# Kernel optimization log

Measured on AMD Instinct MI355X. Metric: run time of the kernel, lower is better.

Reference implementation:

```python
import jax, jax.numpy as jnp
import numpy as np

K = 512          # fixed candidate budget (replaces dynamic torch.where)
THRESH = 0.6
IOU = 0.5
STRIDE = 2.0
OFFSET = 6.0
WIN = 12.0
SCALE = 0.6      # pyramid scale this pass represents (12/min_face_size)


def _conv(x, w, b):
    y = jax.lax.conv_general_dilated(x, w, (1, 1), 'VALID',
                                     dimension_numbers=('NCHW', 'OIHW', 'NCHW'))
    return y + b[None, :, None, None]


def _prelu(x, a):
    return jnp.where(x >= 0, x, a[None, :, None, None] * x)


def _maxpool2(x):
    return jax.lax.reduce_window(x, -jnp.inf, jax.lax.max,
                                 (1, 1, 2, 2), (1, 1, 2, 2), 'VALID')


def _nms(boxes, valid, thr):
    # torchvision-style greedy NMS over score-sorted boxes; `valid` marks live boxes.
    x1, y1, x2, y2 = boxes[:, 0], boxes[:, 1], boxes[:, 2], boxes[:, 3]
    areas = (x2 - x1) * (y2 - y1)
    n = boxes.shape[0]
    idxs = jnp.arange(n)

    def body(i, keep):
        xi1 = jnp.maximum(x1[i], x1); yi1 = jnp.maximum(y1[i], y1)
        xi2 = jnp.minimum(x2[i], x2); yi2 = jnp.minimum(y2[i], y2)
        inter = jnp.clip(xi2 - xi1, 0.0) * jnp.clip(yi2 - yi1, 0.0)
        iou = inter / (areas[i] + areas - inter + 1e-9)
        sup = (iou > thr) & (idxs > i) & keep[i]
        return keep & (~sup)

    return jax.lax.fori_loop(0, n, body, valid)


def setup_inputs() -> dict:
    key = jax.random.key(0)
    ks = jax.random.split(key, 14)
    d = {}
    d['x'] = jax.random.normal(ks[0], (1, 3, 2048, 2048), dtype=jnp.float32)
    d['w1'] = jax.random.normal(ks[1], (10, 3, 3, 3), dtype=jnp.float32) * 0.1
    d['b1'] = jax.random.normal(ks[2], (10,), dtype=jnp.float32) * 0.01
    d['p1'] = jax.random.uniform(ks[3], (10,), dtype=jnp.float32) * 0.25
    d['w2'] = jax.random.normal(ks[4], (16, 10, 3, 3), dtype=jnp.float32) * 0.1
    d['b2'] = jax.random.normal(ks[5], (16,), dtype=jnp.float32) * 0.01
    d['p2'] = jax.random.uniform(ks[6], (16,), dtype=jnp.float32) * 0.25
    d['w3'] = jax.random.normal(ks[7], (32, 16, 3, 3), dtype=jnp.float32) * 0.1
    d['b3'] = jax.random.normal(ks[8], (32,), dtype=jnp.float32) * 0.01
    d['p3'] = jax.random.uniform(ks[9], (32,), dtype=jnp.float32) * 0.25
    d['wa'] = jax.random.normal(ks[10], (2, 32, 1, 1), dtype=jnp.float32) * 0.1
    d['ba'] = jax.random.normal(ks[11], (2,), dtype=jnp.float32) * 0.01
    d['wb'] = jax.random.normal(ks[12], (4, 32, 1, 1), dtype=jnp.float32) * 0.1
    d['bb'] = jax.random.normal(ks[13], (4,), dtype=jnp.float32) * 0.01
    return d


def reference(x, w1, b1, p1, w2, b2, p2, w3, b3, p3, wa, ba, wb, bb):
    H, W = x.shape[2], x.shape[3]
    h = _prelu(_conv(x, w1, b1), p1)
    h = _maxpool2(h)
    h = _prelu(_conv(h, w2, b2), p2)
    h = _prelu(_conv(h, w3, b3), p3)
    cls = _conv(h, wa, ba)              # [1,2,hf,wf]
    reg = _conv(h, wb, bb)              # [1,4,hf,wf]
    prob = jax.nn.softmax(cls, axis=1)[0, 1]   # Softmax2d over channels, face prob
    hf, wf = prob.shape
    scores = prob.reshape(-1)
    regf = jnp.transpose(reg[0], (1, 2, 0)).reshape(-1, 4)
    # threshold gather -> fixed-size top-K with invalid slots at score -1
    masked = jnp.where(scores >= THRESH, scores, -1.0)
    top_s, idx = jax.lax.top_k(masked, K)
    reg_k = regf[idx]
    yy = (idx // wf).astype(jnp.float32)
    xx = (idx % wf).astype(jnp.float32)
    off_x = ((W - OFFSET * 2) % STRIDE) / 2.0 + OFFSET
    off_y = ((H - OFFSET * 2) % STRIDE) / 2.0 + OFFSET
    cx = (xx * STRIDE + off_x) / SCALE
    cy = (yy * STRIDE + off_y) / SCALE
    ww = WIN / SCALE                    # square 12x12 window / scale
    x1 = cx - ww / 2 + reg_k[:, 0] * ww
    y1 = cy - ww / 2 + reg_k[:, 1] * ww
    x2 = cx + ww / 2 + reg_k[:, 2] * ww
    y2 = cy + ww / 2 + reg_k[:, 3] * ww
    boxes = jnp.stack([x1, y1, x2, y2], axis=1)   # [K,4]
    valid = top_s >= THRESH
    keep = _nms(boxes, valid, IOU)                # per-scale NMS
    keep = _nms(boxes, keep, IOU + 0.2)           # final cross-scale NMS
    out = jnp.concatenate([boxes, top_s[:, None]], axis=1)
    return out * keep[:, None].astype(out.dtype)  # [K,5] boxes+score, zeroed if dropped
```

## Files before the change

### kernel.cpp

```cpp
#include <hip/hip_runtime.h>

typedef unsigned long long u64;
typedef unsigned int u32;

#define W1H 1023
#define W2H 1021
#define W3H 1019
#define NPIX (W3H * W3H)
#define IDXMASK 0xFFFFFull
#define PSTR 1024

#define NBINS 2048
#define HLO 0.3055f
#define HW_ 0.025f
#define HINV 40.0f
#define HDELTA 0.10f

#define W1OFF 0
#define B1OFF 270
#define P1OFF 280
#define W2OFF 290
#define B2OFF 1730
#define P2OFF 1746
#define W3OFF 1762
#define B3OFF 6370
#define P3OFF 6402
#define WAOFF 6434
#define BAOFF 6498
#define WBOFF 6500
#define BBOFF 6628
#define WDTOT 6632

__device__ __forceinline__ int xcd_swizzle(int bid, int nwg) {
    int q = nwg >> 3, r = nwg & 7;
    int x = bid & 7, i = bid >> 3;
    return (x < r ? x * (q + 1) : r * (q + 1) + (x - r) * q) + i;
}

__global__ __launch_bounds__(256) void k_prep(
    const float* __restrict__ w1, const float* __restrict__ b1, const float* __restrict__ p1,
    const float* __restrict__ w2, const float* __restrict__ b2, const float* __restrict__ p2,
    const float* __restrict__ w3, const float* __restrict__ b3, const float* __restrict__ p3,
    const float* __restrict__ wa, const float* __restrict__ ba,
    const float* __restrict__ wb, const float* __restrict__ bb,
    double* __restrict__ wd, int* __restrict__ ctrl, u32* __restrict__ ghist)
{
    int t = threadIdx.x;
    if (t < 2) ctrl[t] = 0;
    for (int i = t; i < NBINS; i += 256) ghist[i] = 0u;
    for (int i = t; i < 270; i += 256)  wd[W1OFF + i] = (double)w1[i];
    if (t < 10) { wd[B1OFF + t] = (double)b1[t]; wd[P1OFF + t] = (double)p1[t]; }
    for (int i = t; i < 1440; i += 256) wd[W2OFF + i] = (double)w2[i];
    if (t < 16) { wd[B2OFF + t] = (double)b2[t]; wd[P2OFF + t] = (double)p2[t]; }
    for (int i = t; i < 4608; i += 256) wd[W3OFF + i] = (double)w3[i];
    if (t < 32) { wd[B3OFF + t] = (double)b3[t]; wd[P3OFF + t] = (double)p3[t]; }
    if (t < 64)  wd[WAOFF + t] = (double)wa[t];
    if (t < 2)   wd[BAOFF + t] = (double)ba[t];
    if (t < 128) wd[WBOFF + t] = (double)wb[t];
    if (t < 4)   wd[BBOFF + t] = (double)bb[t];
}

__global__ __launch_bounds__(256) void k_conv1f(
    const float* __restrict__ x, const float* __restrict__ w1,
    const float* __restrict__ b1, const float* __restrict__ p1,
    float* __restrict__ P)
{
    __shared__ float sw[270];
    __shared__ float sb[10], sp[10];
    __shared__ float xs[3][10][132];
    int tx = threadIdx.x, ty = threadIdx.y;
    int t = ty * 64 + tx;
    for (int i = t; i < 270; i += 256) sw[i] = w1[i];
    if (t < 10) { sb[t] = b1[t]; sp[t] = p1[t]; }
    int bx = blockIdx.x, by = blockIdx.y;
    const float4* x4 = (const float4*)x;
    for (int i = t; i < 990; i += 256) {
        int c = i / 330, rem = i % 330, r = rem / 33, k = rem % 33;
        int row = 8 * by + r; if (row > 2047) row = 2047;
        int col4 = bx * 32 + k; if (col4 > 511) col4 = 511;
        float4 v = x4[((size_t)c * 2048 + row) * 512 + col4];
        xs[c][r][k * 4 + 0] = v.x; xs[c][r][k * 4 + 1] = v.y;
        xs[c][r][k * 4 + 2] = v.z; xs[c][r][k * 4 + 3] = v.w;
    }
    __syncthreads();
    int px = bx * 64 + tx;
    int py = by * 4 + ty;
    if (px >= W1H || py >= W1H) return;
    float acc[10][4];
    #pragma unroll
    for (int ch = 0; ch < 10; ++ch) { acc[ch][0]=0.f; acc[ch][1]=0.f; acc[ch][2]=0.f; acc[ch][3]=0.f; }
    for (int c = 0; c < 3; ++c) {
        float in[4][4];
        #pragma unroll
        for (int u = 0; u < 4; ++u) {
            in[u][0] = xs[c][2*ty+u][2*tx+0];
            in[u][1] = xs[c][2*ty+u][2*tx+1];
            in[u][2] = xs[c][2*ty+u][2*tx+2];
            in[u][3] = xs[c][2*ty+u][2*tx+3];
        }
        #pragma unroll
        for (int ch = 0; ch < 10; ++ch) {
            const float* wp = sw + (ch * 3 + c) * 9;
            #pragma unroll
            for (int u = 0; u < 3; ++u)
                #pragma unroll
                for (int v = 0; v < 3; ++v) {
                    float w = wp[u * 3 + v];
                    acc[ch][0] = fmaf(in[u][v],         w, acc[ch][0]);
                    acc[ch][1] = fmaf(in[u][v + 1],     w, acc[ch][1]);
                    acc[ch][2] = fmaf(in[u + 1][v],     w, acc[ch][2]);
                    acc[ch][3] = fmaf(in[u + 1][v + 1], w, acc[ch][3]);
                }
        }
    }
    #pragma unroll
    for (int ch = 0; ch < 10; ++ch) {
        float m = fmaxf(fmaxf(acc[ch][0], acc[ch][1]), fmaxf(acc[ch][2], acc[ch][3])) + sb[ch];
        float r = m >= 0.f ? m : sp[ch] * m;
        P[((size_t)ch * W1H + py) * PSTR + px] = r;
    }
}

__global__ __launch_bounds__(256) void k_conv2f(
    const float* __restrict__ P, const float* __restrict__ w2,
    const float* __restrict__ b2, const float* __restrict__ p2,
    float* __restrict__ H2)
{
    __shared__ __align__(16) float sw[10 * 16 * 12];
    __shared__ float sb[16], sp[16];
    int tx = threadIdx.x, ty = threadIdx.y;
    int t = ty * 64 + tx;
    for (int i = t; i < 1440; i += 256) {
        int o = i / 90, r = i % 90, c = r / 9, k = r % 9;
        sw[(c * 16 + o) * 12 + k] = w2[i];
    }
    if (t < 16) { sb[t] = b2[t]; sp[t] = p2[t]; }
    __syncthreads();
    int py = xcd_swizzle(blockIdx.y, W2H);
    int och0 = (ty & 1) * 8;
    int px_base = (ty >> 1) * 512 + tx * 8;
    float acc[8][8];
    #pragma unroll
    for (int j = 0; j < 8; ++j)
        #pragma unroll
        for (int p = 0; p < 8; ++p) acc[j][p] = 0.f;

    for (int c = 0; c < 10; ++c) {
        float f[3][12];
        #pragma unroll
        for (int u = 0; u < 3; ++u) {
            const float* row = P + ((size_t)c * W1H + (py + u)) * PSTR + px_base;
            float4 a = *(const float4*)(row);
            float4 b = *(const float4*)(row + 4);
            float4 d = *(const float4*)(row + 8);
            f[u][0]=a.x; f[u][1]=a.y; f[u][2]=a.z;  f[u][3]=a.w;
            f[u][4]=b.x; f[u][5]=b.y; f[u][6]=b.z;  f[u][7]=b.w;
            f[u][8]=d.x; f[u][9]=d.y; f[u][10]=d.z; f[u][11]=d.w;
        }
        #pragma unroll
        for (int j = 0; j < 8; ++j) {
            int o = och0 + j;
            const float4* wv = (const float4*)(sw + (c * 16 + o) * 12);
            float4 wA = wv[0], wB = wv[1], wC = wv[2];
            float w[9] = {wA.x,wA.y,wA.z,wA.w,wB.x,wB.y,wB.z,wB.w,wC.x};
            #pragma unroll
            for (int u = 0; u < 3; ++u)
                #pragma unroll
                for (int v = 0; v < 3; ++v) {
                    float wt = w[u*3+v];
                    #pragma unroll
                    for (int p = 0; p < 8; ++p)
                        acc[j][p] = fmaf(f[u][p+v], wt, acc[j][p]);
                }
        }
    }
    #pragma unroll
    for (int j = 0; j < 8; ++j) {
        int o = och0 + j;
        float bb_ = sb[o], pp_ = sp[o];
        #pragma unroll
        for (int p = 0; p < 8; ++p) {
            int px = px_base + p;
            if (px < W2H) {
                float v = acc[j][p] + bb_;
                v = v >= 0.f ? v : pp_ * v;
                H2[((size_t)o * W2H + py) * PSTR + px] = v;
            }
        }
    }
}

__global__ __launch_bounds__(512, 2) void k_conv3f(
    const float* __restrict__ H2, const float* __restrict__ w3,
    const float* __restrict__ b3, const float* __restrict__ p3,
    const float* __restrict__ wa, const float* __restrict__ ba,
    float* __restrict__ Lg, u32* __restrict__ ghist)
{
    __shared__ __align__(16) float sw[16 * 32 * 12];
    __shared__ float spart[4][1024];
    __shared__ u32 hist[NBINS];
    __shared__ float sb[32], sp[32], swd[32];
    __shared__ float slgb;
    int tx = threadIdx.x, ty = threadIdx.y;
    int t = ty * 64 + tx;
    for (int i = t; i < 4608; i += 512) {
        int o = i / 144, rem = i % 144, c = rem / 9, k = rem % 9;
        sw[(c * 32 + o) * 12 + k] = w3[i];
    }
    if (t < 32) { sb[t] = b3[t]; sp[t] = p3[t]; swd[t] = wa[32 + t] - wa[t]; }
    if (t == 0) slgb = ba[1] - ba[0];
    for (int i = t; i < NBINS; i += 512) hist[i] = 0u;
    __syncthreads();

    int py = xcd_swizzle(blockIdx.y, W3H);
    int och0 = (ty & 3) * 8;
    int px_base = (ty >> 2) * 512 + tx * 8;
    float acc[8][8];
    #pragma unroll
    for (int j = 0; j < 8; ++j)
        #pragma unroll
        for (int p = 0; p < 8; ++p) acc[j][p] = 0.f;

    for (int c = 0; c < 16; ++c) {
        float f[3][12];
        #pragma unroll
        for (int u = 0; u < 3; ++u) {
            const float* row = H2 + ((size_t)c * W2H + (py + u)) * PSTR + px_base;
            float4 a = *(const float4*)(row);
            float4 b = *(const float4*)(row + 4);
            float4 d = *(const float4*)(row + 8);
            f[u][0]=a.x; f[u][1]=a.y; f[u][2]=a.z;  f[u][3]=a.w;
            f[u][4]=b.x; f[u][5]=b.y; f[u][6]=b.z;  f[u][7]=b.w;
            f[u][8]=d.x; f[u][9]=d.y; f[u][10]=d.z; f[u][11]=d.w;
        }
        #pragma unroll
        for (int j = 0; j < 8; ++j) {
            int o = och0 + j;
            const float4* wv = (const float4*)(sw + (c * 32 + o) * 12);
            float4 wA = wv[0], wB = wv[1], wC = wv[2];
            float w[9] = {wA.x,wA.y,wA.z,wA.w,wB.x,wB.y,wB.z,wB.w,wC.x};
            #pragma unroll
            for (int u = 0; u < 3; ++u)
                #pragma unroll
                for (int v = 0; v < 3; ++v) {
                    float wt = w[u*3+v];
                    #pragma unroll
                    for (int p = 0; p < 8; ++p)
                        acc[j][p] = fmaf(f[u][p+v], wt, acc[j][p]);
                }
        }
    }

    float partv[8];
    #pragma unroll
    for (int p = 0; p < 8; ++p) partv[p] = 0.f;
    #pragma unroll
    for (int j = 0; j < 8; ++j) {
        int o = och0 + j;
        float bb_ = sb[o], pp_ = sp[o], wdd = swd[o];
        #pragma unroll
        for (int p = 0; p < 8; ++p) {
            float v = acc[j][p] + bb_;
            v = v >= 0.f ? v : pp_ * v;
            partv[p] = fmaf(wdd, v, partv[p]);
        }
    }
    #pragma unroll
    for (int p = 0; p < 8; ++p) spart[ty & 3][px_base + p] = partv[p];
    __syncthreads();

    #pragma unroll
    for (int rep = 0; rep < 2; ++rep) {
        int pl = t + rep * 512;
        float lg = slgb;
        #pragma unroll
        for (int g = 0; g < 4; ++g) lg += spart[g][pl];
        if (pl < W3H) {
            Lg[(size_t)py * W3H + pl] = lg;
            if (lg >= HLO) {
                int bin = (int)((lg - HLO) * HINV);
                if (bin > NBINS - 1) bin = NBINS - 1;
                atomicAdd(&hist[bin], 1u);
            }
        }
    }
    __syncthreads();
    for (int i = t; i < NBINS; i += 512) {
        u32 v = hist[i];
        if (v) atomicAdd(&ghist[i], v);
    }
}

__global__ __launch_bounds__(256) void k_select(
    const float* __restrict__ Lg, const u32* __restrict__ ghist,
    int* __restrict__ ctrl, u32* __restrict__ selidx)
{
    __shared__ u32 h[NBINS];
    __shared__ u32 tsum[256];
    __shared__ int best;
    __shared__ float sT;
    int t = threadIdx.x;
    for (int i = t; i < NBINS; i += 256) h[i] = ghist[i];
    if (t == 0) best = -1;
    __syncthreads();
    u32 s = 0;
    #pragma unroll
    for (int k = 0; k < 8; ++k) s += h[t * 8 + k];
    tsum[t] = s;
    __syncthreads();
    for (int off = 1; off < 256; off <<= 1) {
        u32 add = (t + off < 256) ? tsum[t + off] : 0u;
        __syncthreads();
        tsum[t] += add;
        __syncthreads();
    }
    u32 cum = (t < 255) ? tsum[t + 1] : 0u;
    int cand = -1;
    for (int k = 7; k >= 0; --k) {
        cum += h[t * 8 + k];
        if (cand < 0 && cum >= 512) cand = t * 8 + k;
    }
    if (cand >= 0) atomicMax(&best, cand);
    __syncthreads();
    if (t == 0) sT = (best < 0) ? HLO : (HLO + (float)best * HW_ - HDELTA);
    __syncthreads();
    float T = sT;
    int stride = gridDim.x * 256;
    for (int i = blockIdx.x * 256 + t; i < NPIX; i += stride) {
        if (Lg[i] >= T) {
            int slot = atomicAdd(&ctrl[0], 1);
            selidx[slot] = (u32)i;
        }
    }
}

__global__ __launch_bounds__(64) void k_recomp(
    const float* __restrict__ x, const double* __restrict__ wd,
    const u32* __restrict__ selidx, int* __restrict__ ctrl,
    u64* __restrict__ keys, double* __restrict__ boxplane)
{
    __shared__ double xw[3][12][12];
    __shared__ double Pw[10][5][5];
    __shared__ double Hw[16][3][3];
    __shared__ double vch[32];
    int nsel = ctrl[0]; if (nsel > NPIX) nsel = NPIX;
    int t = threadIdx.x;
    for (int s = blockIdx.x; s < nsel; s += gridDim.x) {
        u32 idx = selidx[s];
        int y3 = (int)(idx / W3H), x3 = (int)(idx % W3H);
        int xr = 2 * y3, xc = 2 * x3;
        for (int i = t; i < 432; i += 64) {
            int c = i / 144, r = (i % 144) / 12, cc = i % 12;
            xw[c][r][cc] = (double)x[((size_t)c * 2048 + (xr + r)) * 2048 + (xc + cc)];
        }
        __syncthreads();
        for (int i = t; i < 250; i += 64) {
            int ch = i / 25, py = (i % 25) / 5, px = i % 5;
            int r0 = py * 2, c0 = px * 2;
            double a00=0.0, a01=0.0, a10=0.0, a11=0.0;
            for (int c = 0; c < 3; ++c) {
                const double* wp = wd + W1OFF + (ch * 3 + c) * 9;
                #pragma unroll
                for (int u = 0; u < 3; ++u)
                    #pragma unroll
                    for (int v = 0; v < 3; ++v) {
                        double w = wp[u * 3 + v];
                        a00 = fma(xw[c][r0+u][c0+v],     w, a00);
                        a01 = fma(xw[c][r0+u][c0+v+1],   w, a01);
                        a10 = fma(xw[c][r0+u+1][c0+v],   w, a10);
                        a11 = fma(xw[c][r0+u+1][c0+v+1], w, a11);
                    }
            }
            double m = fmax(fmax(a00, a01), fmax(a10, a11)) + wd[B1OFF + ch];
            Pw[ch][py][px] = m >= 0.0 ? m : wd[P1OFF + ch] * m;
        }
        __syncthreads();
        for (int i = t; i < 144; i += 64) {
            int o = i / 9, hy = (i % 9) / 3, hx = i % 3;
            double acc = 0.0;
            for (int c = 0; c < 10; ++c) {
                const double* wp = wd + W2OFF + (o * 10 + c) * 9;
                #pragma unroll
                for (int k = 0; k < 9; ++k)
                    acc = fma(Pw[c][hy + k / 3][hx + k % 3], wp[k], acc);
            }
            acc += wd[B2OFF + o];
            Hw[o][hy][hx] = acc >= 0.0 ? acc : wd[P2OFF + o] * acc;
        }
        __syncthreads();
        if (t < 32) {
            double acc = 0.0;
            for (int c = 0; c < 16; ++c) {
                const double* wp = wd + W3OFF + (t * 16 + c) * 9;
                #pragma unroll
                for (int k = 0; k < 9; ++k)
                    acc = fma(Hw[c][k / 3][k % 3], wp[k], acc);
            }
            acc += wd[B3OFF + t];
            vch[t] = acc >= 0.0 ? acc : wd[P3OFF + t] * acc;
        }
        __syncthreads();
        if (t == 0) {
            double c0 = wd[BAOFF + 0], c1 = wd[BAOFF + 1];
            for (int o = 0; o < 32; ++o) {
                c0 = fma(wd[WAOFF + o], vch[o], c0);
                c1 = fma(wd[WAOFF + 32 + o], vch[o], c1);
            }
            double mx = fmax(c0, c1);
            double e0 = exp(c0 - mx), e1 = exp(c1 - mx);
            double prob = e1 / (e0 + e1);
            if (prob >= 0.6) {
                double r0 = wd[BBOFF+0], r1 = wd[BBOFF+1], r2 = wd[BBOFF+2], r3 = wd[BBOFF+3];
                for (int o = 0; o < 32; ++o) {
                    double v = vch[o];
                    r0 = fma(wd[WBOFF + o], v, r0);
                    r1 = fma(wd[WBOFF + 32 + o], v, r1);
                    r2 = fma(wd[WBOFF + 64 + o], v, r2);
                    r3 = fma(wd[WBOFF + 96 + o], v, r3);
                }
                double fx = (double)x3, fy = (double)y3;
                double cx = (fx * 2.0 + 6.0) / 0.6;
                double cy = (fy * 2.0 + 6.0) / 0.6;
                double ww = 12.0 / 0.6, hw = ww / 2.0;
                double* bp = boxplane + (size_t)idx * 5;
                bp[0] = cx - hw + r0 * ww;
                bp[1] = cy - hw + r1 * ww;
                bp[2] = cx + hw + r2 * ww;
                bp[3] = cy + hw + r3 * ww;
                bp[4] = prob;
                u64 bits = (u64)__double_as_longlong(prob);
                u64 kh = (bits - 0x3FE0000000000000ull) >> 9;
                int slot = atomicAdd(&ctrl[1], 1);
                keys[slot] = (kh << 20) | ((u64)(~idx) & IDXMASK);
            }
        }
        __syncthreads();
    }
}

__global__ __launch_bounds__(512) void k_sortchunks(
    const u64* __restrict__ cand, const int* __restrict__ ctrl,
    u64* __restrict__ sorted)
{
    __shared__ u64 stop_[512];
    __shared__ u64 schunk[512];
    int tid = threadIdx.x;
    int n = ctrl[1]; if (n > NPIX) n = NPIX;
    long base0 = (long)blockIdx.x * 2048;
    stop_[tid] = 0ull;
    if (base0 < n) {
        for (int s = 0; s < 4; ++s) {
            long base = base0 + (long)s * 512;
            if (base >= n) break;
            schunk[tid] = (base + tid < n) ? cand[base + tid] : 0ull;
            for (int k = 2; k <= 512; k <<= 1)
                for (int j = k >> 1; j > 0; j >>= 1) {
                    __syncthreads();
                    int ixj = tid ^ j;
                    if (ixj > tid) {
                        u64 a = schunk[tid], b = schunk[ixj];
                        bool desc = ((tid & k) == 0);
                        if (desc ? (a < b) : (a > b)) { schunk[tid] = b; schunk[ixj] = a; }
                    }
                }
            __syncthreads();
            u64 m = stop_[tid], v = schunk[511 - tid];
            stop_[tid] = m > v ? m : v;
            for (int j = 256; j > 0; j >>= 1) {
                __syncthreads();
                int ixj = tid ^ j;
                if (ixj > tid) {
                    u64 a = stop_[tid], b = stop_[ixj];
                    if (a < b) { stop_[tid] = b; stop_[ixj] = a; }
                }
            }
            __syncthreads();
        }
    }
    sorted[(size_t)blockIdx.x * 512 + tid] = stop_[tid];
}

__global__ __launch_bounds__(512) void k_merge8(
    const u64* __restrict__ in, u64* __restrict__ out, int nin)
{
    __shared__ u64 s[512];
    int tid = threadIdx.x;
    int base = blockIdx.x * 8;
    s[tid] = (base < nin) ? in[(size_t)base * 512 + tid] : 0ull;
    for (int c = 1; c < 8; ++c) {
        int li = base + c;
        u64 v = (li < nin) ? in[(size_t)li * 512 + (511 - tid)] : 0ull;
        __syncthreads();
        u64 m = s[tid];
        s[tid] = m > v ? m : v;
        for (int j = 256; j > 0; j >>= 1) {
            __syncthreads();
            int ixj = tid ^ j;
            if (ixj > tid) {
                u64 a = s[tid], b = s[ixj];
                if (a < b) { s[tid] = b; s[ixj] = a; }
            }
        }
        __syncthreads();
    }
    out[(size_t)blockIdx.x * 512 + tid] = s[tid];
}

__global__ __launch_bounds__(512) void k_boxmat(
    const u64* __restrict__ lists, const double* __restrict__ boxplane,
    u64* __restrict__ mats, double* __restrict__ bxs, u64* __restrict__ validw)
{
    __shared__ double sx1[512], sy1[512], sx2[512], sy2[512], sar[512];
    int tid = threadIdx.x;
    u64 key = lists[tid];
    bool valid = key != 0ull;
    double x1 = 0.0, y1 = 0.0, x2 = 0.0, y2 = 0.0, score = 0.0;
    if (valid) {
        u32 idx = (u32)(IDXMASK - (key & IDXMASK));
        const double* bp = boxplane + (size_t)idx * 5;
        x1 = bp[0]; y1 = bp[1]; x2 = bp[2]; y2 = bp[3]; score = bp[4];
    }
    double area = (x2 - x1) * (y2 - y1);
    sx1[tid] = x1; sy1[tid] = y1; sx2[tid] = x2; sy2[tid] = y2; sar[tid] = area;
    if (blockIdx.x == 0 && blockIdx.y == 0) {
        bxs[tid] = x1; bxs[512 + tid] = y1; bxs[1024 + tid] = x2;
        bxs[1536 + tid] = y2; bxs[2048 + tid] = score;
        u64 bal = __ballot(valid);
        if ((tid & 63) == 0) validw[tid >> 6] = bal;
    }
    __syncthreads();
    double thr = (blockIdx.y == 0) ? 0.5 : 0.7;
    int wv = tid >> 6;
    int rowbase = blockIdx.x * 64;
    for (int r = 0; r < 64; ++r) {
        int i = rowbase + r;
        double ix1 = fmax(sx1[i], x1);
        double iy1 = fmax(sy1[i], y1);
        double ix2 = fmin(sx2[i], x2);
        double iy2 = fmin(sy2[i], y2);
        double inter = fmax(ix2 - ix1, 0.0) * fmax(iy2 - iy1, 0.0);
        double uni = sar[i] + area - inter + 1e-9;
        bool sup = (uni > 0.0) && (inter > thr * uni) && (tid > i);
        u64 w = __ballot(sup);
        if ((tid & 63) == 0)
            mats[((size_t)blockIdx.y * 512 + i) * 8 + wv] = w;
    }
}

__global__ __launch_bounds__(512) void k_nmsfin(
    const u64* __restrict__ mats, const double* __restrict__ bxs,
    const u64* __restrict__ validw, float* __restrict__ out)
{
    __shared__ u64 keepw[8];
    int tid = threadIdx.x;
    if (tid < 8) keepw[tid] = validw[tid];
    __syncthreads();
    for (int pass = 0; pass < 2; ++pass) {
        if (tid < 64) {
            const u64* mat = mats + (size_t)pass * 512 * 8;
            u64 kw = (tid < 8) ? keepw[tid] : 0ull;
            for (int i = 0; i < 512; ++i) {
                u64 row = mat[i * 8 + (tid & 7)];
                u64 cur = __shfl(kw, i >> 6);
                if ((cur >> (i & 63)) & 1) kw &= ~row;
            }
            if (tid < 8) keepw[tid] = kw;
        }
        __syncthreads();
    }
    double kf = ((keepw[tid >> 6] >> (tid & 63)) & 1) ? 1.0 : 0.0;
    out[tid * 5 + 0] = (float)(bxs[tid] * kf);
    out[tid * 5 + 1] = (float)(bxs[512 + tid] * kf);
    out[tid * 5 + 2] = (float)(bxs[1024 + tid] * kf);
    out[tid * 5 + 3] = (float)(bxs[1536 + tid] * kf);
    out[tid * 5 + 4] = (float)(bxs[2048 + tid] * kf);
}

extern "C" void kernel_launch(void* const* d_in, const int* in_sizes, int n_in,
                              void* d_out, int out_size, void* d_ws, size_t ws_size,
                              hipStream_t stream)
{
    const float* x  = (const float*)d_in[0];
    const float* w1 = (const float*)d_in[1];
    const float* b1 = (const float*)d_in[2];
    const float* p1 = (const float*)d_in[3];
    const float* w2 = (const float*)d_in[4];
    const float* b2 = (const float*)d_in[5];
    const float* p2 = (const float*)d_in[6];
    const float* w3 = (const float*)d_in[7];
    const float* b3 = (const float*)d_in[8];
    const float* p3 = (const float*)d_in[9];
    const float* wa = (const float*)d_in[10];
    const float* ba = (const float*)d_in[11];
    const float* wb = (const float*)d_in[12];
    const float* bb = (const float*)d_in[13];
    float* out = (float*)d_out;

    char* ws = (char*)d_ws;
    float*  Pf    = (float*) (ws);
    float*  H2f   = (float*) (ws + 41902080);
    float*  Lg    = (float*) (ws + 108814336);
    u32*    ghist = (u32*)   (ws + 112967936);
    int*    ctrl  = (int*)   (ws + 112976128);
    u32*    selidx= (u32*)   (ws + 112976384);
    u64*    keys  = (u64*)   (ws + 117129984);
    u64*    sorted= (u64*)   (ws + 125437184);
    u64*    l1out = (u64*)   (ws + 127517952);
    u64*    l2out = (u64*)   (ws + 127780096);
    double* boxpl = (double*)(ws + 127812864);
    double* wd    = (double*)(ws + 169347584);
    u64*    l3out = (u64*)   (ws + 125437184);
    u64*    mats  = (u64*)   (ws + 125441280);
    double* bxs   = (double*)(ws + 125506816);
    u64*    vwords= (u64*)   (ws + 125527296);

    k_prep<<<1, 256, 0, stream>>>(w1, b1, p1, w2, b2, p2, w3, b3, p3, wa, ba, wb, bb, wd, ctrl, ghist);
    k_conv1f<<<dim3(16, 256), dim3(64, 4), 0, stream>>>(x, w1, b1, p1, Pf);
    k_conv2f<<<dim3(1, W2H), dim3(64, 4), 0, stream>>>(Pf, w2, b2, p2, H2f);
    k_conv3f<<<dim3(1, W3H), dim3(64, 8), 0, stream>>>(H2f, w3, b3, p3, wa, ba, Lg, ghist);
    k_select<<<1024, 256, 0, stream>>>(Lg, ghist, ctrl, selidx);
    k_recomp<<<2048, 64, 0, stream>>>(x, wd, selidx, ctrl, keys, boxpl);
    k_sortchunks<<<508, 512, 0, stream>>>(keys, ctrl, sorted);
    k_merge8<<<64, 512, 0, stream>>>(sorted, l1out, 508);
    k_merge8<<<8, 512, 0, stream>>>(l1out, l2out, 64);
    k_merge8<<<1, 512, 0, stream>>>(l2out, l3out, 8);
    k_boxmat<<<dim3(8, 2), 512, 0, stream>>>(l3out, boxpl, mats, bxs, vwords);
    k_nmsfin<<<1, 512, 0, stream>>>(mats, bxs, vwords, out);
}
```

Baseline: 584.1 us.

## Collapse top-K sort/merge chain, vectorize select scan, unroll conv channel loops

```diff
diff --git a/kernel.cpp b/kernel.cpp
--- a/kernel.cpp
+++ b/kernel.cpp
@@ -145,6 +145,7 @@
         #pragma unroll
         for (int p = 0; p < 8; ++p) acc[j][p] = 0.f;
 
+    #pragma unroll 2
     for (int c = 0; c < 10; ++c) {
         float f[3][12];
         #pragma unroll
@@ -221,6 +222,7 @@
         #pragma unroll
         for (int p = 0; p < 8; ++p) acc[j][p] = 0.f;
 
+    #pragma unroll 2
     for (int c = 0; c < 16; ++c) {
         float f[3][12];
         #pragma unroll
@@ -326,11 +328,17 @@
     __syncthreads();
     float T = sT;
     int stride = gridDim.x * 256;
-    for (int i = blockIdx.x * 256 + t; i < NPIX; i += stride) {
-        if (Lg[i] >= T) {
-            int slot = atomicAdd(&ctrl[0], 1);
-            selidx[slot] = (u32)i;
-        }
+    const float4* Lg4 = (const float4*)Lg;
+    int n4 = NPIX >> 2;
+    for (int i = blockIdx.x * 256 + t; i < n4; i += stride) {
+        float4 v = Lg4[i];
+        if (v.x >= T) { int s_ = atomicAdd(&ctrl[0], 1); selidx[s_] = (u32)(i * 4 + 0); }
+        if (v.y >= T) { int s_ = atomicAdd(&ctrl[0], 1); selidx[s_] = (u32)(i * 4 + 1); }
+        if (v.z >= T) { int s_ = atomicAdd(&ctrl[0], 1); selidx[s_] = (u32)(i * 4 + 2); }
+        if (v.w >= T) { int s_ = atomicAdd(&ctrl[0], 1); selidx[s_] = (u32)(i * 4 + 3); }
+    }
+    if (blockIdx.x == 0 && t == 0) {
+        if (Lg[NPIX - 1] >= T) { int s_ = atomicAdd(&ctrl[0], 1); selidx[s_] = (u32)(NPIX - 1); }
     }
 }
 
@@ -438,58 +446,54 @@
     }
 }
 
-__global__ __launch_bounds__(512) void k_sortchunks(
-    const u64* __restrict__ cand, const int* __restrict__ ctrl,
-    u64* __restrict__ sorted)
+__global__ __launch_bounds__(512) void k_top8(
+    const u64* __restrict__ keys, const int* __restrict__ ctrl,
+    u64* __restrict__ lists8)
 {
     __shared__ u64 stop_[512];
     __shared__ u64 schunk[512];
     int tid = threadIdx.x;
     int n = ctrl[1]; if (n > NPIX) n = NPIX;
-    long base0 = (long)blockIdx.x * 2048;
+    int nchunks = (n + 511) / 512;
     stop_[tid] = 0ull;
-    if (base0 < n) {
-        for (int s = 0; s < 4; ++s) {
-            long base = base0 + (long)s * 512;
-            if (base >= n) break;
-            schunk[tid] = (base + tid < n) ? cand[base + tid] : 0ull;
-            for (int k = 2; k <= 512; k <<= 1)
-                for (int j = k >> 1; j > 0; j >>= 1) {
-                    __syncthreads();
-                    int ixj = tid ^ j;
-                    if (ixj > tid) {
-                        u64 a = schunk[tid], b = schunk[ixj];
-                        bool desc = ((tid & k) == 0);
-                        if (desc ? (a < b) : (a > b)) { schunk[tid] = b; schunk[ixj] = a; }
-                    }
-                }
-            __syncthreads();
-            u64 m = stop_[tid], v = schunk[511 - tid];
-            stop_[tid] = m > v ? m : v;
-            for (int j = 256; j > 0; j >>= 1) {
+    for (int c = blockIdx.x; c < nchunks; c += 8) {
+        long base = (long)c * 512;
+        schunk[tid] = (base + tid < n) ? keys[base + tid] : 0ull;
+        for (int k = 2; k <= 512; k <<= 1)
+            for (int j = k >> 1; j > 0; j >>= 1) {
                 __syncthreads();
                 int ixj = tid ^ j;
                 if (ixj > tid) {
-                    u64 a = stop_[tid], b = stop_[ixj];
-                    if (a < b) { stop_[tid] = b; stop_[ixj] = a; }
+                    u64 a = schunk[tid], b = schunk[ixj];
+                    bool desc = ((tid & k) == 0);
+                    if (desc ? (a < b) : (a > b)) { schunk[tid] = b; schunk[ixj] = a; }
                 }
             }
+        __syncthreads();
+        u64 m = stop_[tid], v = schunk[511 - tid];
+        stop_[tid] = m > v ? m : v;
+        for (int j = 256; j > 0; j >>= 1) {
             __syncthreads();
-        }
-    }
-    sorted[(size_t)blockIdx.x * 512 + tid] = stop_[tid];
-}
-
-__global__ __launch_bounds__(512) void k_merge8(
-    const u64* __restrict__ in, u64* __restrict__ out, int nin)
+            int ixj = tid ^ j;
+            if (ixj > tid) {
+                u64 a = stop_[tid], b = stop_[ixj];
+                if (a < b) { stop_[tid] = b; stop_[ixj] = a; }
+            }
+        }
+        __syncthreads();
+    }
+    lists8[(size_t)blockIdx.x * 512 + tid] = stop_[tid];
+}
+
+__global__ __launch_bounds__(512) void k_mergefin(
+    const u64* __restrict__ lists8, const double* __restrict__ boxplane,
+    u64* __restrict__ l3out, double* __restrict__ bxs, u64* __restrict__ validw)
 {
     __shared__ u64 s[512];
     int tid = threadIdx.x;
-    int base = blockIdx.x * 8;
-    s[tid] = (base < nin) ? in[(size_t)base * 512 + tid] : 0ull;
+    s[tid] = lists8[tid];
     for (int c = 1; c < 8; ++c) {
-        int li = base + c;
-        u64 v = (li < nin) ? in[(size_t)li * 512 + (511 - tid)] : 0ull;
+        u64 v = lists8[(size_t)c * 512 + (511 - tid)];
         __syncthreads();
         u64 m = s[tid];
         s[tid] = m > v ? m : v;
@@ -503,16 +507,8 @@
         }
         __syncthreads();
     }
-    out[(size_t)blockIdx.x * 512 + tid] = s[tid];
-}
-
-__global__ __launch_bounds__(512) void k_boxmat(
-    const u64* __restrict__ lists, const double* __restrict__ boxplane,
-    u64* __restrict__ mats, double* __restrict__ bxs, u64* __restrict__ validw)
-{
-    __shared__ double sx1[512], sy1[512], sx2[512], sy2[512], sar[512];
-    int tid = threadIdx.x;
-    u64 key = lists[tid];
+    u64 key = s[tid];
+    l3out[tid] = key;
     bool valid = key != 0ull;
     double x1 = 0.0, y1 = 0.0, x2 = 0.0, y2 = 0.0, score = 0.0;
     if (valid) {
@@ -520,14 +516,28 @@
         const double* bp = boxplane + (size_t)idx * 5;
         x1 = bp[0]; y1 = bp[1]; x2 = bp[2]; y2 = bp[3]; score = bp[4];
     }
+    bxs[tid] = x1; bxs[512 + tid] = y1; bxs[1024 + tid] = x2;
+    bxs[1536 + tid] = y2; bxs[2048 + tid] = score;
+    u64 bal = __ballot(valid);
+    if ((tid & 63) == 0) validw[tid >> 6] = bal;
+}
+
+__global__ __launch_bounds__(512) void k_boxmat(
+    const u64* __restrict__ l3out, const double* __restrict__ boxplane,
+    u64* __restrict__ mats)
+{
+    __shared__ double sx1[512], sy1[512], sx2[512], sy2[512], sar[512];
+    int tid = threadIdx.x;
+    u64 key = l3out[tid];
+    bool valid = key != 0ull;
+    double x1 = 0.0, y1 = 0.0, x2 = 0.0, y2 = 0.0;
+    if (valid) {
+        u32 idx = (u32)(IDXMASK - (key & IDXMASK));
+        const double* bp = boxplane + (size_t)idx * 5;
+        x1 = bp[0]; y1 = bp[1]; x2 = bp[2]; y2 = bp[3];
+    }
     double area = (x2 - x1) * (y2 - y1);
     sx1[tid] = x1; sy1[tid] = y1; sx2[tid] = x2; sy2[tid] = y2; sar[tid] = area;
-    if (blockIdx.x == 0 && blockIdx.y == 0) {
-        bxs[tid] = x1; bxs[512 + tid] = y1; bxs[1024 + tid] = x2;
-        bxs[1536 + tid] = y2; bxs[2048 + tid] = score;
-        u64 bal = __ballot(valid);
-        if ((tid & 63) == 0) validw[tid >> 6] = bal;
-    }
     __syncthreads();
     double thr = (blockIdx.y == 0) ? 0.5 : 0.7;
     int wv = tid >> 6;
@@ -604,15 +614,13 @@
     int*    ctrl  = (int*)   (ws + 112976128);
     u32*    selidx= (u32*)   (ws + 112976384);
     u64*    keys  = (u64*)   (ws + 117129984);
-    u64*    sorted= (u64*)   (ws + 125437184);
-    u64*    l1out = (u64*)   (ws + 127517952);
-    u64*    l2out = (u64*)   (ws + 127780096);
+    u64*    lists8= (u64*)   (ws + 125437184);
+    u64*    l3out = (u64*)   (ws + 125469952);
+    u64*    mats  = (u64*)   (ws + 125474048);
+    double* bxs   = (double*)(ws + 125539584);
+    u64*    vwords= (u64*)   (ws + 125560064);
     double* boxpl = (double*)(ws + 127812864);
     double* wd    = (double*)(ws + 169347584);
-    u64*    l3out = (u64*)   (ws + 125437184);
-    u64*    mats  = (u64*)   (ws + 125441280);
-    double* bxs   = (double*)(ws + 125506816);
-    u64*    vwords= (u64*)   (ws + 125527296);
 
     k_prep<<<1, 256, 0, stream>>>(w1, b1, p1, w2, b2, p2, w3, b3, p3, wa, ba, wb, bb, wd, ctrl, ghist);
     k_conv1f<<<dim3(16, 256), dim3(64, 4), 0, stream>>>(x, w1, b1, p1, Pf);
@@ -620,10 +628,8 @@
     k_conv3f<<<dim3(1, W3H), dim3(64, 8), 0, stream>>>(H2f, w3, b3, p3, wa, ba, Lg, ghist);
     k_select<<<1024, 256, 0, stream>>>(Lg, ghist, ctrl, selidx);
     k_recomp<<<2048, 64, 0, stream>>>(x, wd, selidx, ctrl, keys, boxpl);
-    k_sortchunks<<<508, 512, 0, stream>>>(keys, ctrl, sorted);
-    k_merge8<<<64, 512, 0, stream>>>(sorted, l1out, 508);
-    k_merge8<<<8, 512, 0, stream>>>(l1out, l2out, 64);
-    k_merge8<<<1, 512, 0, stream>>>(l2out, l3out, 8);
-    k_boxmat<<<dim3(8, 2), 512, 0, stream>>>(l3out, boxpl, mats, bxs, vwords);
+    k_top8<<<8, 512, 0, stream>>>(keys, ctrl, lists8);
+    k_mergefin<<<1, 512, 0, stream>>>(lists8, boxpl, l3out, bxs, vwords);
+    k_boxmat<<<dim3(8, 2), 512, 0, stream>>>(l3out, boxpl, mats);
     k_nmsfin<<<1, 512, 0, stream>>>(mats, bxs, vwords, out);
 }
```

New measurement: 566.4 us. -3.0%, faster.
